# Performance work log

Hardware: AMD Instinct MI355X
Metric: run time of the kernel (lower is better)

Reference implementation:

```python
import jax, jax.numpy as jnp
import numpy as np

N = 50000   # total nodes
E = 600000  # total edges
F = 128     # in_features == hidden_features
H = 128
L = 4       # layers_count
B = 256     # number of graphs in batch
M = 200     # molecule_features
OUT = 12    # out_features
MH = H // 4 # molecular head width


def setup_inputs() -> dict:
    key = jax.random.key(0)
    ks = jax.random.split(key, 16)
    x = jax.random.normal(ks[0], (N, F), dtype=jnp.float32)
    edge_index = jax.random.randint(ks[1], (2, E), 0, N, dtype=jnp.int64)
    # sorted segment ids; guarantee every graph has >=1 node
    batch = jnp.sort(jnp.concatenate([
        jnp.arange(B, dtype=jnp.int64),
        jax.random.randint(ks[2], (N - B,), 0, B, dtype=jnp.int64)]))
    molecule_features = jax.random.normal(ks[3], (B, M), dtype=jnp.float32)
    s = 0.05
    Ws = jax.random.normal(ks[4], (L, H, H), dtype=jnp.float32) * s
    bs = jnp.zeros((L, H), dtype=jnp.float32)
    Wm = jax.random.normal(ks[5], (M, MH), dtype=jnp.float32) * s
    bm = jnp.zeros((MH,), dtype=jnp.float32)
    gamma = jnp.ones((MH,), dtype=jnp.float32)   # BatchNorm1d affine (eval mode, running stats 0/1)
    beta = jnp.zeros((MH,), dtype=jnp.float32)
    W1 = jax.random.normal(ks[6], (2 * H + MH, H), dtype=jnp.float32) * s  # mlp in = 288
    b1 = jnp.zeros((H,), dtype=jnp.float32)
    W2 = jax.random.normal(ks[7], (H, OUT), dtype=jnp.float32) * s
    b2 = jnp.zeros((OUT,), dtype=jnp.float32)
    return dict(x=x, edge_index=edge_index, batch=batch,
                molecule_features=molecule_features, Ws=Ws, bs=bs,
                Wm=Wm, bm=bm, gamma=gamma, beta=beta,
                W1=W1, b1=b1, W2=W2, b2=b2)


def gcn_conv(x, src, dst, W, b):
    # GCNConv: D^{-1/2} (A + I) D^{-1/2} X W + b, degrees include self loops
    ones = jnp.ones((E,), dtype=x.dtype)
    deg = jax.ops.segment_sum(ones, dst, num_segments=N) + 1.0  # self loop
    dis = jax.lax.rsqrt(deg)
    norm = dis[src] * dis[dst]                      # [E]
    xw = x @ W                                      # [N,H]
    msg = xw[src] * norm[:, None]                   # gather + scale
    agg = jax.ops.segment_sum(msg, dst, num_segments=N)
    agg = agg + xw * (dis * dis)[:, None]           # self-loop term
    return agg + b


def reference(x, edge_index, batch, molecule_features, Ws, bs, Wm, bm,
              gamma, beta, W1, b1, W2, b2):
    src, dst = edge_index[0], edge_index[1]
    h = x
    for l in range(L):
        y = jax.nn.relu(gcn_conv(h, src, dst, Ws[l], bs[l]))
        h = y + h  # residual (in == hidden); dropout is identity in eval
    max_pool = jax.ops.segment_max(h, batch, num_segments=B)
    add_pool = jax.ops.segment_sum(h, batch, num_segments=B)
    # molecular head: Linear -> Dropout(eval=identity) -> BatchNorm1d(eval) -> ReLU
    mol = molecule_features @ Wm + bm
    mol = jax.nn.relu(mol * gamma + beta)  # running_mean=0, running_var=1
    z = jnp.concatenate((max_pool, add_pool, mol), axis=1)  # [B, 288]
    z = jax.nn.relu(z @ W1 + b1)
    return z @ W2 + b2  # [B, OUT]
```

## Files before the change

### kernel.cpp

```cpp
#include <hip/hip_runtime.h>
#include <math.h>

static constexpr int NN  = 50000;
static constexpr int NE  = 600000;
static constexpr int HD  = 128;
static constexpr int NL  = 4;
static constexpr int NB  = 256;
static constexpr int NM  = 200;
static constexpr int NO  = 12;
static constexpr int NMH = 32;

#define MAX4(ac, b) { (ac).x = fmaxf((ac).x,(b).x); (ac).y = fmaxf((ac).y,(b).y); (ac).z = fmaxf((ac).z,(b).z); (ac).w = fmaxf((ac).w,(b).w); }
#define ADD4(ac, b) { (ac).x += (b).x; (ac).y += (b).y; (ac).z += (b).z; (ac).w += (b).w; }

typedef short bfx8 __attribute__((ext_vector_type(8)));
typedef float f32x4 __attribute__((ext_vector_type(4)));

__device__ __forceinline__ unsigned short f2bf(float f) {
  unsigned int u = __float_as_uint(f);
  unsigned int r = (u + 0x7fffu + ((u >> 16) & 1u)) >> 16;
  return (unsigned short)r;
}
__device__ __forceinline__ float bflo(unsigned int p) { return __uint_as_float(p << 16); }
__device__ __forceinline__ float bfhi(unsigned int p) { return __uint_as_float(p & 0xffff0000u); }

__global__ void k_hist(const int* __restrict__ dst, int* __restrict__ counts) {
  int e = blockIdx.x * blockDim.x + threadIdx.x;
  if (e < NE) atomicAdd(&counts[dst[e]], 1);
}

__global__ void k_scan1(const int* __restrict__ counts, int* __restrict__ incl,
                        int* __restrict__ bsum, float* __restrict__ dis) {
  __shared__ int s[256];
  int i = blockIdx.x * 256 + threadIdx.x;
  int v = (i < NN) ? counts[i] : 0;
  if (i < NN) dis[i] = rsqrtf((float)(v + 1));
  s[threadIdx.x] = v;
  __syncthreads();
  for (int off = 1; off < 256; off <<= 1) {
    int t = (threadIdx.x >= off) ? s[threadIdx.x - off] : 0;
    __syncthreads();
    s[threadIdx.x] += t;
    __syncthreads();
  }
  if (i < NN) incl[i] = s[threadIdx.x];
  if (threadIdx.x == 255) bsum[blockIdx.x] = s[255];
}

__global__ void k_scan2(const int* __restrict__ bsum, int* __restrict__ boff, int nblocks) {
  __shared__ int s[256];
  int v = (threadIdx.x < nblocks) ? bsum[threadIdx.x] : 0;
  s[threadIdx.x] = v;
  __syncthreads();
  for (int off = 1; off < 256; off <<= 1) {
    int t = (threadIdx.x >= off) ? s[threadIdx.x - off] : 0;
    __syncthreads();
    s[threadIdx.x] += t;
    __syncthreads();
  }
  boff[threadIdx.x] = s[threadIdx.x] - v;
}

__global__ void k_scan3(const int* __restrict__ counts, int* __restrict__ rowst, const int* __restrict__ boff) {
  int i = blockIdx.x * 256 + threadIdx.x;
  if (i < NN) {
    rowst[i] = rowst[i] - counts[i] + boff[blockIdx.x];
    if (i == NN - 1) rowst[NN] = NE;
  }
}

__global__ void k_fill(const int* __restrict__ src, const int* __restrict__ dst,
                       const int* __restrict__ rowst, const float* __restrict__ dis,
                       int* __restrict__ cur, uint2* __restrict__ csr) {
  int e = blockIdx.x * blockDim.x + threadIdx.x;
  if (e < NE) {
    int d = dst[e];
    int s = src[e];
    int p = atomicAdd(&cur[d], 1);
    csr[rowst[d] + p] = make_uint2((unsigned)s, __float_as_uint(dis[s]));
  }
}

__global__ void k_goffs(const int* __restrict__ batch, int* __restrict__ goffs) {
  int i = blockIdx.x * blockDim.x + threadIdx.x;
  if (i >= NN) return;
  int b = batch[i];
  if (i == 0) {
    for (int g = 0; g <= b; ++g) goffs[g] = 0;
  } else {
    int pb = batch[i - 1];
    for (int g = pb + 1; g <= b; ++g) goffs[g] = i;
  }
  if (i == NN - 1) goffs[NB] = NN;
}

__global__ void k_tobf(const float4* __restrict__ in, ushort4* __restrict__ outb, int n4) {
  int i = blockIdx.x * blockDim.x + threadIdx.x;
  if (i < n4) {
    float4 v = in[i];
    outb[i] = make_ushort4(f2bf(v.x), f2bf(v.y), f2bf(v.z), f2bf(v.w));
  }
}

__global__ void k_wT(const float* __restrict__ Ws, unsigned short* __restrict__ wT) {
  int i = blockIdx.x * blockDim.x + threadIdx.x;
  if (i < NL * HD * HD) {
    int l = i >> 14, rem = i & 16383, n = rem >> 7, k = rem & 127;
    wT[i] = f2bf(Ws[l * 16384 + k * 128 + n]);
  }
}

__launch_bounds__(256)
__global__ void k_gemm_mfma(const unsigned short* __restrict__ A,
                            const unsigned short* __restrict__ WT,
                            unsigned short* __restrict__ C) {
  const int wave = threadIdx.x >> 6;
  const int lane = threadIdx.x & 63;
  const int m_base = blockIdx.x * 128 + wave * 32;
  const int lr = lane & 15;
  const int kg = lane >> 4;

  f32x4 acc[2][8];
#pragma unroll
  for (int mi = 0; mi < 2; ++mi)
#pragma unroll
    for (int nj = 0; nj < 8; ++nj) acc[mi][nj] = (f32x4){0.f, 0.f, 0.f, 0.f};

  int ra0 = m_base + lr;       if (ra0 > NN - 1) ra0 = NN - 1;
  int ra1 = m_base + 16 + lr;  if (ra1 > NN - 1) ra1 = NN - 1;

#pragma unroll
  for (int kb = 0; kb < 4; ++kb) {
    const int k0 = kb * 32 + kg * 8;
    bfx8 a0 = *(const bfx8*)&A[(size_t)ra0 * HD + k0];
    bfx8 a1 = *(const bfx8*)&A[(size_t)ra1 * HD + k0];
#pragma unroll
    for (int nj = 0; nj < 8; ++nj) {
      bfx8 b = *(const bfx8*)&WT[(nj * 16 + lr) * HD + k0];
      acc[0][nj] = __builtin_amdgcn_mfma_f32_16x16x32_bf16(a0, b, acc[0][nj], 0, 0, 0);
      acc[1][nj] = __builtin_amdgcn_mfma_f32_16x16x32_bf16(a1, b, acc[1][nj], 0, 0, 0);
    }
  }

  const int col = lane & 15;
  const int rbase = (lane >> 4) * 4;
#pragma unroll
  for (int mi = 0; mi < 2; ++mi) {
#pragma unroll
    for (int r = 0; r < 4; ++r) {
      int row = m_base + mi * 16 + rbase + r;
      if (row < NN) {
#pragma unroll
        for (int nj = 0; nj < 8; ++nj) {
          C[(size_t)row * HD + nj * 16 + col] = f2bf(acc[mi][nj][r]);
        }
      }
    }
  }
}

__global__ void k_agg(const unsigned short* __restrict__ xw, const float* __restrict__ dis,
                      const int* __restrict__ rowst, const uint2* __restrict__ csr,
                      const float* __restrict__ bias, const unsigned short* __restrict__ hinb,
                      unsigned short* __restrict__ houtb) {
  int g = threadIdx.x >> 5;
  int lane = threadIdx.x & 31;
  int n = blockIdx.x * 8 + g;
  if (n >= NN) return;

  const uint2* xwb = (const uint2*)xw;

  float dn = dis[n];
  float4 acc;
  {
    uint2 p = xwb[(size_t)n * 32 + lane];
    float sl = dn * dn;
    acc.x = bflo(p.x) * sl; acc.y = bfhi(p.x) * sl;
    acc.z = bflo(p.y) * sl; acc.w = bfhi(p.y) * sl;
  }

  int s0 = rowst[n], s1 = rowst[n + 1];
  int idx = s0;
  for (; idx + 4 <= s1; idx += 4) {
    uint2 eA = csr[idx], eB = csr[idx + 1], eC = csr[idx + 2], eD = csr[idx + 3];
    uint2 pA = xwb[(size_t)eA.x * 32 + lane];
    uint2 pB = xwb[(size_t)eB.x * 32 + lane];
    uint2 pC = xwb[(size_t)eC.x * 32 + lane];
    uint2 pD = xwb[(size_t)eD.x * 32 + lane];
    float nA = __uint_as_float(eA.y) * dn;
    float nB = __uint_as_float(eB.y) * dn;
    float nC = __uint_as_float(eC.y) * dn;
    float nD = __uint_as_float(eD.y) * dn;
    acc.x += nA * bflo(pA.x); acc.y += nA * bfhi(pA.x);
    acc.z += nA * bflo(pA.y); acc.w += nA * bfhi(pA.y);
    acc.x += nB * bflo(pB.x); acc.y += nB * bfhi(pB.x);
    acc.z += nB * bflo(pB.y); acc.w += nB * bfhi(pB.y);
    acc.x += nC * bflo(pC.x); acc.y += nC * bfhi(pC.x);
    acc.z += nC * bflo(pC.y); acc.w += nC * bfhi(pC.y);
    acc.x += nD * bflo(pD.x); acc.y += nD * bfhi(pD.x);
    acc.z += nD * bflo(pD.y); acc.w += nD * bfhi(pD.y);
  }
  for (; idx < s1; ++idx) {
    uint2 eA = csr[idx];
    uint2 pA = xwb[(size_t)eA.x * 32 + lane];
    float nA = __uint_as_float(eA.y) * dn;
    acc.x += nA * bflo(pA.x); acc.y += nA * bfhi(pA.x);
    acc.z += nA * bflo(pA.y); acc.w += nA * bfhi(pA.y);
  }

  float4 b4 = *(const float4*)&bias[lane * 4];
  uint2 hp = ((const uint2*)hinb)[(size_t)n * 32 + lane];
  float4 outv;
  outv.x = fmaxf(acc.x + b4.x, 0.f) + bflo(hp.x);
  outv.y = fmaxf(acc.y + b4.y, 0.f) + bfhi(hp.x);
  outv.z = fmaxf(acc.z + b4.z, 0.f) + bflo(hp.y);
  outv.w = fmaxf(acc.w + b4.w, 0.f) + bfhi(hp.y);
  *(ushort4*)&houtb[(size_t)n * HD + lane * 4] =
      make_ushort4(f2bf(outv.x), f2bf(outv.y), f2bf(outv.z), f2bf(outv.w));
}

__launch_bounds__(1024)
__global__ void k_pool(const unsigned short* __restrict__ hb, const int* __restrict__ goffs,
                       float* __restrict__ pooled) {
  __shared__ float4 smax[32][32];
  __shared__ float4 ssum[32][32];
  int g = blockIdx.x;
  int slot = threadIdx.x >> 5;
  int lane = threadIdx.x & 31;
  int a = goffs[g], bnd = goffs[g + 1];
  const uint2* hb2 = (const uint2*)hb;

  float4 mx = make_float4(-INFINITY, -INFINITY, -INFINITY, -INFINITY);
  float4 sm = make_float4(0.f, 0.f, 0.f, 0.f);
  for (int i = a + slot; i < bnd; i += 32) {
    uint2 p = hb2[(size_t)i * 32 + lane];
    float4 v = make_float4(bflo(p.x), bfhi(p.x), bflo(p.y), bfhi(p.y));
    MAX4(mx, v);
    ADD4(sm, v);
  }
  smax[slot][lane] = mx;
  ssum[slot][lane] = sm;
  __syncthreads();
#pragma unroll
  for (int off = 16; off >= 1; off >>= 1) {
    if (slot < off) {
      float4 m2 = smax[slot + off][lane];
      float4 s2 = ssum[slot + off][lane];
      float4 m1 = smax[slot][lane];
      float4 s1 = ssum[slot][lane];
      MAX4(m1, m2);
      ADD4(s1, s2);
      smax[slot][lane] = m1;
      ssum[slot][lane] = s1;
    }
    __syncthreads();
  }
  if (slot == 0) {
    *(float4*)&pooled[g * 256 + lane * 4]       = smax[0][lane];
    *(float4*)&pooled[g * 256 + 128 + lane * 4] = ssum[0][lane];
  }
}

__global__ void k_head(const float* __restrict__ pooled, const float* __restrict__ mf,
                       const float* __restrict__ Wm, const float* __restrict__ bm,
                       const float* __restrict__ gamma, const float* __restrict__ beta,
                       const float* __restrict__ W1, const float* __restrict__ b1,
                       const float* __restrict__ W2, const float* __restrict__ b2,
                       float* __restrict__ out) {
  __shared__ float z[288];
  __shared__ float z1[128];
  int g = blockIdx.x, t = threadIdx.x;
  z[t] = pooled[g * 256 + t];
  z[128 + t] = pooled[g * 256 + 128 + t];
  if (t < NMH) {
    float acc = bm[t];
    for (int k = 0; k < NM; ++k) acc += mf[g * NM + k] * Wm[k * NMH + t];
    acc = acc * gamma[t] + beta[t];
    z[256 + t] = fmaxf(acc, 0.f);
  }
  __syncthreads();
  float acc = b1[t];
  for (int k = 0; k < 288; ++k) acc += z[k] * W1[k * HD + t];
  z1[t] = fmaxf(acc, 0.f);
  __syncthreads();
  if (t < NO) {
    float a2 = b2[t];
    for (int k = 0; k < HD; ++k) a2 += z1[k] * W2[k * NO + t];
    out[g * NO + t] = a2;
  }
}

extern "C" void kernel_launch(void* const* d_in, const int* in_sizes, int n_in,
                              void* d_out, int out_size, void* d_ws, size_t ws_size,
                              hipStream_t stream) {
  const float* x     = (const float*)d_in[0];
  const int*   eidx  = (const int*)d_in[1];
  const int*   batch = (const int*)d_in[2];
  const float* mf    = (const float*)d_in[3];
  const float* Ws    = (const float*)d_in[4];
  const float* bs    = (const float*)d_in[5];
  const float* Wm    = (const float*)d_in[6];
  const float* bm    = (const float*)d_in[7];
  const float* gamma = (const float*)d_in[8];
  const float* beta  = (const float*)d_in[9];
  const float* W1    = (const float*)d_in[10];
  const float* b1    = (const float*)d_in[11];
  const float* W2    = (const float*)d_in[12];
  const float* b2    = (const float*)d_in[13];
  float* out = (float*)d_out;

  const int* src = eidx;
  const int* dst = eidx + NE;

  char* w = (char*)d_ws;
  size_t off = 0;
  auto alloc = [&](size_t bytes) -> void* {
    void* p = w + off;
    off += (bytes + 255) & ~(size_t)255;
    return p;
  };
  float* dis    = (float*)alloc((size_t)NN * 4);
  unsigned short* xw  = (unsigned short*)alloc((size_t)NN * HD * 2);
  unsigned short* xbf = (unsigned short*)alloc((size_t)NN * HD * 2);
  unsigned short* hbf = (unsigned short*)alloc((size_t)NN * HD * 2);
  unsigned short* wT  = (unsigned short*)alloc((size_t)NL * HD * HD * 2);
  int* counts   = (int*)alloc((size_t)NN * 4);
  int* cur      = (int*)alloc((size_t)NN * 4);
  int* rowst    = (int*)alloc((size_t)(NN + 1) * 4);
  uint2* csr    = (uint2*)alloc((size_t)NE * 8);
  int* bsum     = (int*)alloc(256 * 4);
  int* boff     = (int*)alloc(256 * 4);
  int* goffs    = (int*)alloc((size_t)(NB + 1) * 4);
  float* pooled = (float*)alloc((size_t)NB * 256 * 4);
  (void)ws_size;

  const int SB = (NN + 255) / 256;

  hipMemsetAsync(counts, 0, (size_t)NN * 4, stream);
  hipMemsetAsync(cur, 0, (size_t)NN * 4, stream);

  k_hist<<<(NE + 255) / 256, 256, 0, stream>>>(dst, counts);
  k_scan1<<<SB, 256, 0, stream>>>(counts, rowst, bsum, dis);
  k_scan2<<<1, 256, 0, stream>>>(bsum, boff, SB);
  k_scan3<<<SB, 256, 0, stream>>>(counts, rowst, boff);
  k_fill<<<(NE + 255) / 256, 256, 0, stream>>>(src, dst, rowst, dis, cur, csr);

  k_goffs<<<SB, 256, 0, stream>>>(batch, goffs);
  k_tobf<<<((NN * HD / 4) + 255) / 256, 256, 0, stream>>>((const float4*)x, (ushort4*)xbf, NN * HD / 4);
  k_wT<<<(NL * HD * HD + 255) / 256, 256, 0, stream>>>(Ws, wT);

  for (int l = 0; l < NL; ++l) {
    const unsigned short* gin_bf = (l == 0) ? xbf : hbf;
    k_gemm_mfma<<<(NN + 127) / 128, 256, 0, stream>>>(gin_bf, wT + (size_t)l * HD * HD, xw);
    k_agg<<<(NN + 7) / 8, 256, 0, stream>>>(xw, dis, rowst, csr, bs + (size_t)l * HD, gin_bf, hbf);
  }

  k_pool<<<NB, 1024, 0, stream>>>(hbf, goffs, pooled);
  k_head<<<NB, 128, 0, stream>>>(pooled, mf, Wm, bm, gamma, beta, W1, b1, W2, b2, out);
}
```

Baseline: 291.5 us.

## Pack CSR entries into 32 bits with fp16 norm and unroll gather by eight

Each CSR entry shrinks from a uint2 (index plus float norm) to one 32-bit word holding a 16-bit source index and an fp16 norm factor, halving CSR traffic in the fill and the aggregation kernels. The aggregation loop is also unrolled to eight edges to keep more gathers in flight. Source indices up to 49999 fit in 16 bits, and fp16 cuts the norm's precision.

```diff
diff --git a/kernel.cpp b/kernel.cpp
--- a/kernel.cpp
+++ b/kernel.cpp
@@ -1,4 +1,5 @@
 #include <hip/hip_runtime.h>
+#include <hip/hip_fp16.h>
 #include <math.h>
 
 static constexpr int NN  = 50000;
@@ -23,6 +24,9 @@
 }
 __device__ __forceinline__ float bflo(unsigned int p) { return __uint_as_float(p << 16); }
 __device__ __forceinline__ float bfhi(unsigned int p) { return __uint_as_float(p & 0xffff0000u); }
+__device__ __forceinline__ float h2f_hi(unsigned e) {
+  return __half2float(__ushort_as_half((unsigned short)(e >> 16)));
+}
 
 __global__ void k_hist(const int* __restrict__ dst, int* __restrict__ counts) {
   int e = blockIdx.x * blockDim.x + threadIdx.x;
@@ -71,13 +75,14 @@
 
 __global__ void k_fill(const int* __restrict__ src, const int* __restrict__ dst,
                        const int* __restrict__ rowst, const float* __restrict__ dis,
-                       int* __restrict__ cur, uint2* __restrict__ csr) {
+                       int* __restrict__ cur, unsigned* __restrict__ csr) {
   int e = blockIdx.x * blockDim.x + threadIdx.x;
   if (e < NE) {
     int d = dst[e];
     int s = src[e];
     int p = atomicAdd(&cur[d], 1);
-    csr[rowst[d] + p] = make_uint2((unsigned)s, __float_as_uint(dis[s]));
+    unsigned hb = (unsigned)__half_as_ushort(__float2half(dis[s]));
+    csr[rowst[d] + p] = (hb << 16) | (unsigned)s;
   }
 }
 
@@ -159,8 +164,12 @@
   }
 }
 
+#define AGG_EDGE(e, p) { float nm = h2f_hi(e) * dn; \
+    acc.x += nm * bflo((p).x); acc.y += nm * bfhi((p).x); \
+    acc.z += nm * bflo((p).y); acc.w += nm * bfhi((p).y); }
+
 __global__ void k_agg(const unsigned short* __restrict__ xw, const float* __restrict__ dis,
-                      const int* __restrict__ rowst, const uint2* __restrict__ csr,
+                      const int* __restrict__ rowst, const unsigned* __restrict__ csr,
                       const float* __restrict__ bias, const unsigned short* __restrict__ hinb,
                       unsigned short* __restrict__ houtb) {
   int g = threadIdx.x >> 5;
@@ -181,31 +190,32 @@
 
   int s0 = rowst[n], s1 = rowst[n + 1];
   int idx = s0;
+  for (; idx + 8 <= s1; idx += 8) {
+    unsigned e0 = csr[idx],     e1 = csr[idx + 1], e2 = csr[idx + 2], e3 = csr[idx + 3];
+    unsigned e4 = csr[idx + 4], e5 = csr[idx + 5], e6 = csr[idx + 6], e7 = csr[idx + 7];
+    uint2 p0 = xwb[(size_t)(e0 & 0xffffu) * 32 + lane];
+    uint2 p1 = xwb[(size_t)(e1 & 0xffffu) * 32 + lane];
+    uint2 p2 = xwb[(size_t)(e2 & 0xffffu) * 32 + lane];
+    uint2 p3 = xwb[(size_t)(e3 & 0xffffu) * 32 + lane];
+    uint2 p4 = xwb[(size_t)(e4 & 0xffffu) * 32 + lane];
+    uint2 p5 = xwb[(size_t)(e5 & 0xffffu) * 32 + lane];
+    uint2 p6 = xwb[(size_t)(e6 & 0xffffu) * 32 + lane];
+    uint2 p7 = xwb[(size_t)(e7 & 0xffffu) * 32 + lane];
+    AGG_EDGE(e0, p0); AGG_EDGE(e1, p1); AGG_EDGE(e2, p2); AGG_EDGE(e3, p3);
+    AGG_EDGE(e4, p4); AGG_EDGE(e5, p5); AGG_EDGE(e6, p6); AGG_EDGE(e7, p7);
+  }
   for (; idx + 4 <= s1; idx += 4) {
-    uint2 eA = csr[idx], eB = csr[idx + 1], eC = csr[idx + 2], eD = csr[idx + 3];
-    uint2 pA = xwb[(size_t)eA.x * 32 + lane];
-    uint2 pB = xwb[(size_t)eB.x * 32 + lane];
-    uint2 pC = xwb[(size_t)eC.x * 32 + lane];
-    uint2 pD = xwb[(size_t)eD.x * 32 + lane];
-    float nA = __uint_as_float(eA.y) * dn;
-    float nB = __uint_as_float(eB.y) * dn;
-    float nC = __uint_as_float(eC.y) * dn;
-    float nD = __uint_as_float(eD.y) * dn;
-    acc.x += nA * bflo(pA.x); acc.y += nA * bfhi(pA.x);
-    acc.z += nA * bflo(pA.y); acc.w += nA * bfhi(pA.y);
-    acc.x += nB * bflo(pB.x); acc.y += nB * bfhi(pB.x);
-    acc.z += nB * bflo(pB.y); acc.w += nB * bfhi(pB.y);
-    acc.x += nC * bflo(pC.x); acc.y += nC * bfhi(pC.x);
-    acc.z += nC * bflo(pC.y); acc.w += nC * bfhi(pC.y);
-    acc.x += nD * bflo(pD.x); acc.y += nD * bfhi(pD.x);
-    acc.z += nD * bflo(pD.y); acc.w += nD * bfhi(pD.y);
+    unsigned e0 = csr[idx], e1 = csr[idx + 1], e2 = csr[idx + 2], e3 = csr[idx + 3];
+    uint2 p0 = xwb[(size_t)(e0 & 0xffffu) * 32 + lane];
+    uint2 p1 = xwb[(size_t)(e1 & 0xffffu) * 32 + lane];
+    uint2 p2 = xwb[(size_t)(e2 & 0xffffu) * 32 + lane];
+    uint2 p3 = xwb[(size_t)(e3 & 0xffffu) * 32 + lane];
+    AGG_EDGE(e0, p0); AGG_EDGE(e1, p1); AGG_EDGE(e2, p2); AGG_EDGE(e3, p3);
   }
   for (; idx < s1; ++idx) {
-    uint2 eA = csr[idx];
-    uint2 pA = xwb[(size_t)eA.x * 32 + lane];
-    float nA = __uint_as_float(eA.y) * dn;
-    acc.x += nA * bflo(pA.x); acc.y += nA * bfhi(pA.x);
-    acc.z += nA * bflo(pA.y); acc.w += nA * bfhi(pA.y);
+    unsigned e0 = csr[idx];
+    uint2 p0 = xwb[(size_t)(e0 & 0xffffu) * 32 + lane];
+    AGG_EDGE(e0, p0);
   }
 
   float4 b4 = *(const float4*)&bias[lane * 4];
@@ -327,7 +337,7 @@
   int* counts   = (int*)alloc((size_t)NN * 4);
   int* cur      = (int*)alloc((size_t)NN * 4);
   int* rowst    = (int*)alloc((size_t)(NN + 1) * 4);
-  uint2* csr    = (uint2*)alloc((size_t)NE * 8);
+  unsigned* csr = (unsigned*)alloc((size_t)NE * 4);
   int* bsum     = (int*)alloc(256 * 4);
   int* boff     = (int*)alloc(256 * 4);
   int* goffs    = (int*)alloc((size_t)(NB + 1) * 4);
```

After: 283.0 us. -2.9%, faster.
